# Kernel tuning notes

Measured on AMD Instinct MI355X. Metric: run time of the kernel, lower is better.

The kernel has to match this reference:

```python
import jax, jax.numpy as jnp
import numpy as np
import math

B, NV, L = 64, 21, 2048
PATCH, STRIDE = 16, 8
PNUM = (L - PATCH) // STRIDE + 1  # 255 patches
D, H, NDIM = 128, 256, 2
PRED = 96
EPS = 1e-5
SCALE = 1.0 / math.sqrt(NDIM)  # MultiHeadEMA scale = sqrt(1/ndim)
# patch gather indices: [PNUM, PATCH]
PIDX = np.arange(PNUM)[:, None] * STRIDE + np.arange(PATCH)[None, :]


def setup_inputs() -> dict:
    key = jax.random.key(0)
    ks = jax.random.split(key, 24)
    nrm = lambda k, shape, std: std * jax.random.normal(k, shape, jnp.float32)
    inp = {}
    inp['x'] = jax.random.normal(ks[0], (B, NV, L), jnp.float32)
    # LEMencoder feature_projection: LEMblock(PATCH -> H -> D)
    inp['fp_w1'] = nrm(ks[1], (PATCH, H), 0.1)
    inp['fp_b1'] = jnp.zeros((H,), jnp.float32)
    inp['fp_w2'] = nrm(ks[2], (H, D), 0.1)
    inp['fp_b2'] = jnp.zeros((D,), jnp.float32)
    inp['fp_wr'] = nrm(ks[3], (PATCH, D), 0.1)
    inp['fp_br'] = jnp.zeros((D,), jnp.float32)
    inp['fp_g'] = jnp.ones((D,), jnp.float32)
    inp['fp_be'] = jnp.zeros((D,), jnp.float32)
    # 2 stacked encoder LEMblocks (D -> D -> D), leading layer axis
    inp['enc_w1'] = nrm(ks[4], (2, D, D), 0.05)
    inp['enc_b1'] = jnp.zeros((2, D), jnp.float32)
    inp['enc_w2'] = nrm(ks[5], (2, D, D), 0.05)
    inp['enc_b2'] = jnp.zeros((2, D), jnp.float32)
    inp['enc_wr'] = nrm(ks[6], (2, D, D), 0.05)
    inp['enc_br'] = jnp.zeros((2, D), jnp.float32)
    inp['enc_g'] = jnp.ones((2, D), jnp.float32)
    inp['enc_be'] = jnp.zeros((2, D), jnp.float32)
    # MultiHeadEMA params (unidirectional: kernel_dim == D)
    inp['ema_delta'] = nrm(ks[7], (D, NDIM, 1), 0.2)
    inp['ema_alpha'] = nrm(ks[8], (D, NDIM, 1), 0.2)
    val = jnp.array([1.0, -1.0], jnp.float32).reshape(1, NDIM, 1)  # +1/-1 alternating init
    inp['ema_beta'] = nrm(ks[9], (D, NDIM, 1), 0.02) + val
    inp['ema_gamma'] = nrm(ks[10], (D, NDIM), 1.0)
    inp['ema_omega'] = nrm(ks[11], (D,), 1.0)
    # Flatten_Head (shared): Linear(D*PNUM -> PRED)
    inp['head_w'] = nrm(ks[12], (D * PNUM, PRED), 0.02)
    inp['head_b'] = jnp.zeros((PRED,), jnp.float32)
    return inp


def _lemblock(x, w1, b1, w2, b2, wr, br, g, be):
    h = jax.nn.relu(x @ w1 + b1) @ w2 + b2
    y = h + (x @ wr + br)
    mu = jnp.mean(y, axis=-1, keepdims=True)
    var = jnp.mean(jnp.square(y - mu), axis=-1, keepdims=True)
    return g * (y - mu) * jax.lax.rsqrt(var + EPS) + be


def reference(x, fp_w1, fp_b1, fp_w2, fp_b2, fp_wr, fp_br, fp_g, fp_be,
              enc_w1, enc_b1, enc_w2, enc_b2, enc_wr, enc_br, enc_g, enc_be,
              ema_delta, ema_alpha, ema_beta, ema_gamma, ema_omega,
              head_w, head_b):
    # patching: [B, NV, L] -> [B*NV, PNUM, PATCH]
    z = x[:, :, PIDX].reshape(B * NV, PNUM, PATCH)
    # LEMencoder
    z = _lemblock(z, fp_w1, fp_b1, fp_w2, fp_b2, fp_wr, fp_br, fp_g, fp_be)
    for i in range(enc_w1.shape[0]):
        z = _lemblock(z, enc_w1[i], enc_b1[i], enc_w2[i], enc_b2[i],
                      enc_wr[i], enc_br[i], enc_g[i], enc_be[i])
    # MultiHeadEMA over patch (time) axis; input [Time=PNUM, Batch=B*NV, Channel=D]
    t = jnp.transpose(z, (1, 0, 2))
    residual = t * ema_omega
    xc = jnp.transpose(t, (1, 2, 0))  # [BN, D, PNUM]
    p = jax.nn.sigmoid(ema_delta)           # [D, N, 1]
    q = 1.0 - p * jax.nn.sigmoid(ema_alpha)  # [D, N, 1]
    vander = jnp.arange(PNUM, dtype=jnp.float32)[None, None, :] * jnp.log(q)  # [D, N, PNUM]
    kern = p * ema_beta * jnp.exp(vander)
    k = jnp.einsum('dnl,dn->dl', kern, ema_gamma * SCALE)  # [D, PNUM]
    n2 = 2 * PNUM
    out = jnp.fft.irfft(jnp.fft.rfft(xc, n=n2) * jnp.fft.rfft(k, n=n2), n=n2)[..., :PNUM]
    out = jax.nn.silu(jnp.transpose(out, (2, 0, 1)) + residual)  # [PNUM, BN, D]
    # Flatten_Head (shared): [B, NV, D, PNUM] -> flatten(-2) -> linear
    u = jnp.transpose(out, (1, 2, 0)).reshape(B, NV, D * PNUM)
    return u @ head_w + head_b  # [B, NV, PRED]
```

## Files before the change

kernel.cpp:

```cpp
#include <hip/hip_runtime.h>

typedef unsigned short u16;
typedef short bf8v __attribute__((ext_vector_type(8)));
typedef float f4v __attribute__((ext_vector_type(4)));
typedef float f16v __attribute__((ext_vector_type(16)));

#define DEV static __device__ __forceinline__

constexpr int BB   = 64;
constexpr int NV   = 21;
constexpr int BN   = BB * NV;
constexpr int PNUM = 255;
constexpr int D    = 128;
constexpr int PRED = 96;
constexpr int ROWS = BN * PNUM;
constexpr int KH   = D * PNUM;
constexpr int CH   = 30;
constexpr int KPC  = KH / CH;
constexpr int HITER = KPC / 32;
constexpr float EMA_SCALE = 0.70710678118654752440f;

DEV float bf2f(u16 h) { return __uint_as_float(((unsigned)h) << 16); }
DEV u16 f2bf(float f) {
  unsigned u = __float_as_uint(f);
  return (u16)((u + 0x7fffu + ((u >> 16) & 1u)) >> 16);
}
DEV unsigned pkbf2(float a, float b) {
  unsigned ua = __float_as_uint(a) + 0x8000u;
  unsigned ub = __float_as_uint(b) + 0x8000u;
  return __builtin_amdgcn_perm(ub, ua, 0x07060302u);
}
DEV bf8v mk4(unsigned a, unsigned b, unsigned c, unsigned d) {
  int4 t = {(int)a, (int)b, (int)c, (int)d};
  bf8v r;
  __builtin_memcpy(&r, &t, 16);
  return r;
}
DEV bf8v ld8(const u16* p) {
  bf8v r;
  __builtin_memcpy(&r, p, 16);
  return r;
}
DEV f4v mfma16(bf8v a, bf8v b, f4v c) {
  return __builtin_amdgcn_mfma_f32_16x16x32_bf16(a, b, c, 0, 0, 0);
}
DEV f16v mfma32(bf8v a, bf8v b, f16v c) {
  return __builtin_amdgcn_mfma_f32_32x32x16_bf16(a, b, c, 0, 0, 0);
}
DEV f16v zero16() {
  f16v r;
#pragma unroll
  for (int i = 0; i < 16; i++) r[i] = 0.f;
  return r;
}

DEV bf8v frag_pl(unsigned x0, unsigned y0, unsigned x1, unsigned y1) {
  asm("v_permlane32_swap_b32 %0, %1" : "+v"(x0), "+v"(y0));
  asm("v_permlane32_swap_b32 %0, %1" : "+v"(x1), "+v"(y1));
  return mk4(x0, x1, y0, y1);
}
#define FRAG_PL(pk, ks)                                                        \
  frag_pl(pk[(ks) >> 1][2 * ((ks) & 1)][0],                                    \
          pk[(ks) >> 1][2 * ((ks) & 1) + 1][0],                                \
          pk[(ks) >> 1][2 * ((ks) & 1)][1],                                    \
          pk[(ks) >> 1][2 * ((ks) & 1) + 1][1])

__global__ void swz_all(
    const float* __restrict__ fw1, const float* __restrict__ fw2,
    const float* __restrict__ fwr, const float* __restrict__ ew1,
    const float* __restrict__ ew2, const float* __restrict__ ewr,
    const float* __restrict__ hw, u16* __restrict__ wb, u16* __restrict__ wsh) {
  int b = blockIdx.x;
  if (b >= 560) {
    int i = (b - 560) * 256 + threadIdx.x;
    if (i >= KH * PRED) return;
    int kp = i / PRED, n = i - kp * PRED;
    int l = kp >> 7, d = kp & 127;
    wsh[((size_t)(kp >> 3) * PRED + n) * 8 + (kp & 7)] =
        f2bf(hw[(size_t)(d * PNUM + l) * PRED + n]);
    return;
  }
  const float* src; u16* dst; int K, N, Kp;
  if (b < 32)       { src = fw1; dst = wb;          K = 16;  N = 256; Kp = 32; }
  else if (b < 160) { b -= 32;  src = fw2; dst = wb + 8192;  K = 256; N = 128; Kp = 256; }
  else if (b < 176) { b -= 160; src = fwr; dst = wb + 40960; K = 16;  N = 128; Kp = 32; }
  else {
    int e = (b - 176) >> 6; b = (b - 176) & 63;
    int l = e / 3, w = e - 3 * l;
    const float* basep = (w == 0) ? ew1 : (w == 1) ? ew2 : ewr;
    src = basep + (size_t)l * 16384;
    dst = wb + 45056 + e * 16384;
    K = 128; N = 128; Kp = 128;
  }
  int i = b * 256 + threadIdx.x;
  if (i >= Kp * N) return;
  int k = i / N, n = i - k * N;
  u16 v = (k < K) ? f2bf(src[(size_t)k * N + n]) : (u16)0;
  dst[((size_t)(k >> 3) * N + n) * 8 + (k & 7)] = v;
}

__global__ __launch_bounds__(128, 2) void k_lem(
    const float* __restrict__ x,
    const u16* __restrict__ ws1, const float* __restrict__ b1,
    const u16* __restrict__ ws2, const u16* __restrict__ wsr,
    const float* __restrict__ b2, const float* __restrict__ br,
    const float* __restrict__ g, const float* __restrict__ be,
    const u16* __restrict__ wse, const float* __restrict__ eb1,
    const float* __restrict__ eb2, const float* __restrict__ ebr,
    const float* __restrict__ eg, const float* __restrict__ ebe,
    u16* __restrict__ zout) {
  __shared__ __align__(16) u16 zst[64 * 132];
  const int t = threadIdx.x;
  const int lane = t & 63, w = t >> 6;
  const int hh = lane >> 5, r5 = lane & 31;
  const int tile = blockIdx.x;
  const int row = tile * 64 + w * 32 + r5;

  bf8v azv;
  {
    unsigned R = (unsigned)row;
    unsigned bn = R / 255u;
    unsigned p = R - bn * 255u;
    const float* px = x + (size_t)bn * 2048u + p * 8u + hh * 8;
    float4 v0 = *(const float4*)px;
    float4 v1 = *(const float4*)(px + 4);
    azv = mk4(pkbf2(v0.x, v0.y), pkbf2(v0.z, v0.w),
              pkbf2(v1.x, v1.y), pkbf2(v1.z, v1.w));
  }

  unsigned hpk[8][4][2];
  unsigned zpk[4][4][2];

#pragma unroll
  for (int half = 0; half < 2; half++) {
    f16v a[4];
#pragma unroll
    for (int gg = 0; gg < 4; gg++) {
      bf8v wf = ld8(ws1 + ((size_t)(hh * 256 + (half * 4 + gg) * 32 + r5)) * 8);
      a[gg] = mfma32(wf, azv, zero16());
    }
#pragma unroll
    for (int gg = 0; gg < 4; gg++)
#pragma unroll
      for (int wq = 0; wq < 4; wq++) {
        int c0 = (half * 4 + gg) * 32 + wq * 8 + 4 * hh;
        float4 bv = *(const float4*)(b1 + c0);
        float v0 = fmaxf(a[gg][wq * 4 + 0] + bv.x, 0.f);
        float v1 = fmaxf(a[gg][wq * 4 + 1] + bv.y, 0.f);
        float v2 = fmaxf(a[gg][wq * 4 + 2] + bv.z, 0.f);
        float v3 = fmaxf(a[gg][wq * 4 + 3] + bv.w, 0.f);
        hpk[half * 4 + gg][wq][0] = pkbf2(v0, v1);
        hpk[half * 4 + gg][wq][1] = pkbf2(v2, v3);
      }
  }

  {
    f16v acc[4];
#pragma unroll
    for (int gg = 0; gg < 4; gg++) acc[gg] = zero16();
    bf8v wq[3][4];
#pragma unroll
    for (int gg = 0; gg < 4; gg++)
      wq[0][gg] = ld8(wsr + ((size_t)(hh * 128 + gg * 32 + r5)) * 8);
#pragma unroll
    for (int gg = 0; gg < 4; gg++)
      wq[1][gg] = ld8(ws2 + ((size_t)(hh * 128 + gg * 32 + r5)) * 8);
    bf8v bf_cur = azv;
#pragma unroll
    for (int s = 0; s < 17; s++) {
      if (s + 2 < 17) {
        int ks = s + 1;
#pragma unroll
        for (int gg = 0; gg < 4; gg++)
          wq[(s + 2) % 3][gg] =
              ld8(ws2 + ((size_t)((2 * ks + hh) * 128 + gg * 32 + r5)) * 8);
      }
      bf8v bf_nxt = bf_cur;
      if (s + 1 < 17) bf_nxt = FRAG_PL(hpk, s);
#pragma unroll
      for (int gg = 0; gg < 4; gg++) acc[gg] = mfma32(wq[s % 3][gg], bf_cur, acc[gg]);
      bf_cur = bf_nxt;
    }
    float s = 0.f, s2 = 0.f;
#pragma unroll
    for (int gg = 0; gg < 4; gg++)
#pragma unroll
      for (int wq4 = 0; wq4 < 4; wq4++) {
        int c0 = gg * 32 + wq4 * 8 + 4 * hh;
        float4 bv2 = *(const float4*)(b2 + c0);
        float4 bvr = *(const float4*)(br + c0);
        acc[gg][wq4 * 4 + 0] += bv2.x + bvr.x;
        acc[gg][wq4 * 4 + 1] += bv2.y + bvr.y;
        acc[gg][wq4 * 4 + 2] += bv2.z + bvr.z;
        acc[gg][wq4 * 4 + 3] += bv2.w + bvr.w;
#pragma unroll
        for (int sidx = 0; sidx < 4; sidx++) {
          float v = acc[gg][wq4 * 4 + sidx];
          s += v; s2 += v * v;
        }
      }
    s += __shfl_xor(s, 32, 64); s2 += __shfl_xor(s2, 32, 64);
    float mean = s * (1.f / 128.f);
    float rstd = rsqrtf(s2 * (1.f / 128.f) - mean * mean + 1e-5f);
#pragma unroll
    for (int gg = 0; gg < 4; gg++)
#pragma unroll
      for (int wq4 = 0; wq4 < 4; wq4++) {
        int c0 = gg * 32 + wq4 * 8 + 4 * hh;
        float4 gv = *(const float4*)(g + c0);
        float4 bv = *(const float4*)(be + c0);
        float v0 = (acc[gg][wq4 * 4 + 0] - mean) * rstd * gv.x + bv.x;
        float v1 = (acc[gg][wq4 * 4 + 1] - mean) * rstd * gv.y + bv.y;
        float v2 = (acc[gg][wq4 * 4 + 2] - mean) * rstd * gv.z + bv.z;
        float v3 = (acc[gg][wq4 * 4 + 3] - mean) * rstd * gv.w + bv.w;
        zpk[gg][wq4][0] = pkbf2(v0, v1);
        zpk[gg][wq4][1] = pkbf2(v2, v3);
      }
  }

#pragma unroll 1
  for (int L = 0; L < 2; L++) {
    const u16* w1p = wse + (size_t)(L * 3 + 0) * 16384;
    const u16* w2p = wse + (size_t)(L * 3 + 1) * 16384;
    const u16* wrp = wse + (size_t)(L * 3 + 2) * 16384;
    unsigned hp2[4][4][2];
    {
      f16v a2[4];
#pragma unroll
      for (int gg = 0; gg < 4; gg++) a2[gg] = zero16();
      bf8v wq[3][4];
#pragma unroll
      for (int gg = 0; gg < 4; gg++)
        wq[0][gg] = ld8(w1p + ((size_t)(hh * 128 + gg * 32 + r5)) * 8);
#pragma unroll
      for (int gg = 0; gg < 4; gg++)
        wq[1][gg] = ld8(w1p + ((size_t)((2 + hh) * 128 + gg * 32 + r5)) * 8);
      bf8v bf_cur = FRAG_PL(zpk, 0);
#pragma unroll
      for (int s = 0; s < 8; s++) {
        if (s + 2 < 8) {
#pragma unroll
          for (int gg = 0; gg < 4; gg++)
            wq[(s + 2) % 3][gg] =
                ld8(w1p + ((size_t)((2 * (s + 2) + hh) * 128 + gg * 32 + r5)) * 8);
        }
        bf8v bf_nxt = bf_cur;
        if (s + 1 < 8) bf_nxt = FRAG_PL(zpk, s + 1);
#pragma unroll
        for (int gg = 0; gg < 4; gg++) a2[gg] = mfma32(wq[s % 3][gg], bf_cur, a2[gg]);
        bf_cur = bf_nxt;
      }
#pragma unroll
      for (int gg = 0; gg < 4; gg++)
#pragma unroll
        for (int wq4 = 0; wq4 < 4; wq4++) {
          int c0 = gg * 32 + wq4 * 8 + 4 * hh;
          float4 bv = *(const float4*)(eb1 + L * 128 + c0);
          float v0 = fmaxf(a2[gg][wq4 * 4 + 0] + bv.x, 0.f);
          float v1 = fmaxf(a2[gg][wq4 * 4 + 1] + bv.y, 0.f);
          float v2 = fmaxf(a2[gg][wq4 * 4 + 2] + bv.z, 0.f);
          float v3 = fmaxf(a2[gg][wq4 * 4 + 3] + bv.w, 0.f);
          hp2[gg][wq4][0] = pkbf2(v0, v1);
          hp2[gg][wq4][1] = pkbf2(v2, v3);
        }
    }
    f16v acc[4];
#pragma unroll
    for (int gg = 0; gg < 4; gg++) acc[gg] = zero16();
    {
      bf8v wq[3][4];
#pragma unroll
      for (int gg = 0; gg < 4; gg++)
        wq[0][gg] = ld8(w2p + ((size_t)(hh * 128 + gg * 32 + r5)) * 8);
#pragma unroll
      for (int gg = 0; gg < 4; gg++)
        wq[1][gg] = ld8(w2p + ((size_t)((2 + hh) * 128 + gg * 32 + r5)) * 8);
      bf8v bf_cur = FRAG_PL(hp2, 0);
#pragma unroll
      for (int s = 0; s < 16; s++) {
        if (s + 2 < 16) {
          int k2 = s + 2;
          const u16* wp = (k2 < 8) ? w2p : wrp;
          int kk = (k2 < 8) ? k2 : k2 - 8;
#pragma unroll
          for (int gg = 0; gg < 4; gg++)
            wq[k2 % 3][gg] =
                ld8(wp + ((size_t)((2 * kk + hh) * 128 + gg * 32 + r5)) * 8);
        }
        bf8v bf_nxt = bf_cur;
        if (s + 1 < 16) {
          int k1 = s + 1;
          bf_nxt = (k1 < 8) ? FRAG_PL(hp2, k1) : FRAG_PL(zpk, k1 - 8);
        }
#pragma unroll
        for (int gg = 0; gg < 4; gg++) acc[gg] = mfma32(wq[s % 3][gg], bf_cur, acc[gg]);
        bf_cur = bf_nxt;
      }
    }
    float s = 0.f, s2 = 0.f;
#pragma unroll
    for (int gg = 0; gg < 4; gg++)
#pragma unroll
      for (int wq4 = 0; wq4 < 4; wq4++) {
        int c0 = gg * 32 + wq4 * 8 + 4 * hh;
        float4 bv2 = *(const float4*)(eb2 + L * 128 + c0);
        float4 bvr = *(const float4*)(ebr + L * 128 + c0);
        acc[gg][wq4 * 4 + 0] += bv2.x + bvr.x;
        acc[gg][wq4 * 4 + 1] += bv2.y + bvr.y;
        acc[gg][wq4 * 4 + 2] += bv2.z + bvr.z;
        acc[gg][wq4 * 4 + 3] += bv2.w + bvr.w;
#pragma unroll
        for (int sidx = 0; sidx < 4; sidx++) {
          float v = acc[gg][wq4 * 4 + sidx];
          s += v; s2 += v * v;
        }
      }
    s += __shfl_xor(s, 32, 64); s2 += __shfl_xor(s2, 32, 64);
    float mean = s * (1.f / 128.f);
    float rstd = rsqrtf(s2 * (1.f / 128.f) - mean * mean + 1e-5f);
#pragma unroll
    for (int gg = 0; gg < 4; gg++)
#pragma unroll
      for (int wq4 = 0; wq4 < 4; wq4++) {
        int c0 = gg * 32 + wq4 * 8 + 4 * hh;
        float4 gv = *(const float4*)(eg + L * 128 + c0);
        float4 bv = *(const float4*)(ebe + L * 128 + c0);
        float v0 = (acc[gg][wq4 * 4 + 0] - mean) * rstd * gv.x + bv.x;
        float v1 = (acc[gg][wq4 * 4 + 1] - mean) * rstd * gv.y + bv.y;
        float v2 = (acc[gg][wq4 * 4 + 2] - mean) * rstd * gv.z + bv.z;
        float v3 = (acc[gg][wq4 * 4 + 3] - mean) * rstd * gv.w + bv.w;
        unsigned plo = pkbf2(v0, v1), phi = pkbf2(v2, v3);
        if (L == 0) {
          zpk[gg][wq4][0] = plo;
          zpk[gg][wq4][1] = phi;
        } else {
          uint2 pv = {plo, phi};
          *(uint2*)(zst + (w * 32 + r5) * 132 + c0) = pv;
        }
      }
  }

#pragma unroll
  for (int it = 0; it < 8; it++) {
    int lu = it * 64 + lane;
    int rr = lu >> 4, seg = lu & 15;
    int orow = w * 32 + rr;
    *(uint4*)(zout + ((size_t)tile * 64 + orow) * 128 + seg * 8) =
        *(const uint4*)(zst + orow * 132 + seg * 8);
  }
}

__global__ __launch_bounds__(128) void k_ema(
    u16* __restrict__ z,
    const float* __restrict__ pdel, const float* __restrict__ palp,
    const float* __restrict__ pbet, const float* __restrict__ pgam,
    const float* __restrict__ pome) {
  __shared__ __align__(16) u16 zc[64 * 128];
  const int t = threadIdx.x;
  const int bn = blockIdx.x;
  float p0 = 1.f / (1.f + __expf(-pdel[t * 2 + 0]));
  float p1 = 1.f / (1.f + __expf(-pdel[t * 2 + 1]));
  float q0 = 1.f - p0 / (1.f + __expf(-palp[t * 2 + 0]));
  float q1 = 1.f - p1 / (1.f + __expf(-palp[t * 2 + 1]));
  float w0 = p0 * pbet[t * 2 + 0] * pgam[t * 2 + 0] * EMA_SCALE;
  float w1 = p1 * pbet[t * 2 + 1] * pgam[t * 2 + 1] * EMA_SCALE;
  float om = pome[t];
  float s0 = 0.f, s1 = 0.f;
  u16* slab = z + (size_t)bn * KH;

  for (int ch = 0; ch < 4; ch++) {
    int nrow = (ch < 3) ? 64 : 63;
    int nval = nrow * 128;
    for (int i = t * 8; i < nval; i += 128 * 8)
      *(uint4*)(zc + i) = *(const uint4*)(slab + ch * 8192 + i);
    __syncthreads();
    for (int j0 = 0; j0 < nrow; j0 += 8) {
      float xs[8];
#pragma unroll
      for (int jj = 0; jj < 8; jj++)
        if (j0 + jj < nrow) xs[jj] = bf2f(zc[(j0 + jj) * 128 + t]);
#pragma unroll
      for (int jj = 0; jj < 8; jj++)
        if (j0 + jj < nrow) {
          float xv = xs[jj];
          s0 = q0 * s0 + xv;
          s1 = q1 * s1 + xv;
          float v = w0 * s0 + w1 * s1 + om * xv;
          xs[jj] = v / (1.f + __expf(-v));
        }
#pragma unroll
      for (int jj = 0; jj < 8; jj++)
        if (j0 + jj < nrow)
          zc[(j0 + jj) * 128 + t] = (u16)((__float_as_uint(xs[jj]) + 0x8000u) >> 16);
    }
    __syncthreads();
    for (int i = t * 8; i < nval; i += 128 * 8)
      *(uint4*)(slab + ch * 8192 + i) = *(const uint4*)(zc + i);
    __syncthreads();
  }
}

__global__ __launch_bounds__(256) void k_head(
    const u16* __restrict__ u, const u16* __restrict__ whs, float* __restrict__ part) {
  const int t = threadIdx.x;
  const int lane = t & 63, wid = t >> 6;
  const int quad = lane >> 4, lc = lane & 15;
  const int tile = blockIdx.x;
  const int ch = blockIdx.y;
  const int m0 = tile * 64 + wid * 16;
  const u16* Ab = u + (size_t)(m0 + lc) * KH + (size_t)ch * KPC;
  const int g0 = ch * (KPC / 8);
  f4v acc[6];
#pragma unroll
  for (int n = 0; n < 6; n++) acc[n] = (f4v){0.f, 0.f, 0.f, 0.f};
  bf8v a_nxt = ld8(Ab + quad * 8);
  bf8v b_nxt[6];
#pragma unroll
  for (int n = 0; n < 6; n++)
    b_nxt[n] = ld8(whs + ((size_t)(g0 + quad) * PRED + n * 16 + lc) * 8);
  for (int ks = 0; ks < HITER; ks++) {
    bf8v a_cur = a_nxt;
    bf8v b_cur[6];
#pragma unroll
    for (int n = 0; n < 6; n++) b_cur[n] = b_nxt[n];
    if (ks < HITER - 1) {
      a_nxt = ld8(Ab + (ks + 1) * 32 + quad * 8);
#pragma unroll
      for (int n = 0; n < 6; n++)
        b_nxt[n] = ld8(whs + ((size_t)(g0 + (ks + 1) * 4 + quad) * PRED + n * 16 + lc) * 8);
    }
#pragma unroll
    for (int n = 0; n < 6; n++) acc[n] = mfma16(a_cur, b_cur[n], acc[n]);
  }
#pragma unroll
  for (int n = 0; n < 6; n++) {
    int col = n * 16 + lc;
#pragma unroll
    for (int r = 0; r < 4; r++)
      part[((size_t)ch * BN + m0 + quad * 4 + r) * PRED + col] = acc[n][r];
  }
}

__global__ __launch_bounds__(256) void k_red(
    const float* __restrict__ part, const float* __restrict__ hb, float* __restrict__ out) {
  int i = blockIdx.x * 256 + threadIdx.x;
  if (i >= BN * PRED) return;
  int row = i / PRED, col = i - row * PRED;
  float s = hb[col];
#pragma unroll 5
  for (int c = 0; c < CH; c++) s += part[((size_t)c * BN + row) * PRED + col];
  out[i] = s;
}

extern "C" void kernel_launch(void* const* d_in, const int* in_sizes, int n_in,
                              void* d_out, int out_size, void* d_ws, size_t ws_size,
                              hipStream_t stream) {
  const float* x      = (const float*)d_in[0];
  const float* fp_w1  = (const float*)d_in[1];
  const float* fp_b1  = (const float*)d_in[2];
  const float* fp_w2  = (const float*)d_in[3];
  const float* fp_b2  = (const float*)d_in[4];
  const float* fp_wr  = (const float*)d_in[5];
  const float* fp_br  = (const float*)d_in[6];
  const float* fp_g   = (const float*)d_in[7];
  const float* fp_be  = (const float*)d_in[8];
  const float* enc_w1 = (const float*)d_in[9];
  const float* enc_b1 = (const float*)d_in[10];
  const float* enc_w2 = (const float*)d_in[11];
  const float* enc_b2 = (const float*)d_in[12];
  const float* enc_wr = (const float*)d_in[13];
  const float* enc_br = (const float*)d_in[14];
  const float* enc_g  = (const float*)d_in[15];
  const float* enc_be = (const float*)d_in[16];
  const float* e_del  = (const float*)d_in[17];
  const float* e_alp  = (const float*)d_in[18];
  const float* e_bet  = (const float*)d_in[19];
  const float* e_gam  = (const float*)d_in[20];
  const float* e_om   = (const float*)d_in[21];
  const float* head_w = (const float*)d_in[22];
  const float* head_b = (const float*)d_in[23];

  char* base = (char*)d_ws;
  u16* z3 = (u16*)base;
  const size_t EZB = (size_t)ROWS * 128 * 2;
  float* part = (float*)(base + EZB);
  const size_t PARTB = (size_t)CH * BN * PRED * 4;
  u16* wb = (u16*)(base + EZB + PARTB);
  u16* ws1 = wb;
  u16* ws2 = wb + 8192;
  u16* wsr = wb + 40960;
  u16* wse = wb + 45056;
  u16* wsh = wb + 143360;

  swz_all<<<560 + (KH * PRED + 255) / 256, 256, 0, stream>>>(
      fp_w1, fp_w2, fp_wr, enc_w1, enc_w2, enc_wr, head_w, wb, wsh);

  k_lem<<<ROWS / 64, 128, 0, stream>>>(x, ws1, fp_b1, ws2, wsr, fp_b2, fp_br, fp_g, fp_be,
                                       wse, enc_b1, enc_b2, enc_br, enc_g, enc_be, z3);
  k_ema<<<BN, 128, 0, stream>>>(z3, e_del, e_alp, e_bet, e_gam, e_om);
  k_head<<<dim3(21, CH), 256, 0, stream>>>(z3, wsh, part);
  k_red<<<(BN * PRED + 255) / 256, 256, 0, stream>>>(part, head_b, (float*)d_out);
}
```

Before: 397.5 us.

## Stream hidden activations through MLP chunks to cut registers and raise occupancy

Reorders each LEM block so that the first-layer hidden activations are computed one 32-column chunk at a time and fed straight into the second GEMM. The full hidden tile no longer has to stay in registers, and the residual projection is issued first into the shared accumulator. This lets launch bounds rise from 2 to 3 blocks per CU. LayerNorm reductions now use partial sums combined through permlane32 swaps instead of shuffles. The trade-off is that the triple-buffered weight prefetch pipeline is gone, so load latency is exposed more directly.

Measured after the change: 528.3 us. 32.9% more time.

```diff
diff --git a/kernel.cpp b/kernel.cpp
--- a/kernel.cpp
+++ b/kernel.cpp
@@ -59,11 +59,12 @@
   asm("v_permlane32_swap_b32 %0, %1" : "+v"(x1), "+v"(y1));
   return mk4(x0, x1, y0, y1);
 }
-#define FRAG_PL(pk, ks)                                                        \
-  frag_pl(pk[(ks) >> 1][2 * ((ks) & 1)][0],                                    \
-          pk[(ks) >> 1][2 * ((ks) & 1) + 1][0],                                \
-          pk[(ks) >> 1][2 * ((ks) & 1)][1],                                    \
-          pk[(ks) >> 1][2 * ((ks) & 1) + 1][1])
+
+DEV float xadd32(float v) {
+  unsigned a = __float_as_uint(v), b = a;
+  asm("v_permlane32_swap_b32 %0, %1" : "+v"(a), "+v"(b));
+  return __uint_as_float(a) + __uint_as_float(b);
+}
 
 __global__ void swz_all(
     const float* __restrict__ fw1, const float* __restrict__ fw2,
@@ -99,7 +100,7 @@
   dst[((size_t)(k >> 3) * N + n) * 8 + (k & 7)] = v;
 }
 
-__global__ __launch_bounds__(128, 2) void k_lem(
+__global__ __launch_bounds__(128, 3) void k_lem(
     const float* __restrict__ x,
     const u16* __restrict__ ws1, const float* __restrict__ b1,
     const u16* __restrict__ ws2, const u16* __restrict__ wsr,
@@ -128,62 +129,49 @@
               pkbf2(v1.x, v1.y), pkbf2(v1.z, v1.w));
   }
 
-  unsigned hpk[8][4][2];
+  f16v acc[4];
   unsigned zpk[4][4][2];
-
-#pragma unroll
-  for (int half = 0; half < 2; half++) {
-    f16v a[4];
+  bf8v zfr[8];
+
+  {
+#pragma unroll
+    for (int gg = 0; gg < 4; gg++)
+      acc[gg] = mfma32(ld8(wsr + ((size_t)(hh * 128 + gg * 32 + r5)) * 8), azv,
+                       zero16());
+#pragma unroll
+    for (int gq = 0; gq < 8; gq++) {
+      bf8v w2x[4], w2y[4];
+#pragma unroll
+      for (int gg = 0; gg < 4; gg++)
+        w2x[gg] = ld8(ws2 + ((size_t)((4 * gq + hh) * 128 + gg * 32 + r5)) * 8);
+#pragma unroll
+      for (int gg = 0; gg < 4; gg++)
+        w2y[gg] = ld8(ws2 + ((size_t)((4 * gq + 2 + hh) * 128 + gg * 32 + r5)) * 8);
+      bf8v w1f = ld8(ws1 + ((size_t)(hh * 256 + gq * 32 + r5)) * 8);
+      f16v hv = mfma32(w1f, azv, zero16());
+      unsigned hq[4][2];
+#pragma unroll
+      for (int wq = 0; wq < 4; wq++) {
+        int c0 = gq * 32 + wq * 8 + 4 * hh;
+        float4 bv = *(const float4*)(b1 + c0);
+        float v0 = fmaxf(hv[wq * 4 + 0] + bv.x, 0.f);
+        float v1 = fmaxf(hv[wq * 4 + 1] + bv.y, 0.f);
+        float v2 = fmaxf(hv[wq * 4 + 2] + bv.z, 0.f);
+        float v3 = fmaxf(hv[wq * 4 + 3] + bv.w, 0.f);
+        hq[wq][0] = pkbf2(v0, v1);
+        hq[wq][1] = pkbf2(v2, v3);
+      }
+      bf8v f0 = frag_pl(hq[0][0], hq[1][0], hq[0][1], hq[1][1]);
+      bf8v f1 = frag_pl(hq[2][0], hq[3][0], hq[2][1], hq[3][1]);
+#pragma unroll
+      for (int gg = 0; gg < 4; gg++) acc[gg] = mfma32(w2x[gg], f0, acc[gg]);
+#pragma unroll
+      for (int gg = 0; gg < 4; gg++) acc[gg] = mfma32(w2y[gg], f1, acc[gg]);
+    }
+    float sa[4], qa[4];
 #pragma unroll
     for (int gg = 0; gg < 4; gg++) {
-      bf8v wf = ld8(ws1 + ((size_t)(hh * 256 + (half * 4 + gg) * 32 + r5)) * 8);
-      a[gg] = mfma32(wf, azv, zero16());
-    }
-#pragma unroll
-    for (int gg = 0; gg < 4; gg++)
-#pragma unroll
-      for (int wq = 0; wq < 4; wq++) {
-        int c0 = (half * 4 + gg) * 32 + wq * 8 + 4 * hh;
-        float4 bv = *(const float4*)(b1 + c0);
-        float v0 = fmaxf(a[gg][wq * 4 + 0] + bv.x, 0.f);
-        float v1 = fmaxf(a[gg][wq * 4 + 1] + bv.y, 0.f);
-        float v2 = fmaxf(a[gg][wq * 4 + 2] + bv.z, 0.f);
-        float v3 = fmaxf(a[gg][wq * 4 + 3] + bv.w, 0.f);
-        hpk[half * 4 + gg][wq][0] = pkbf2(v0, v1);
-        hpk[half * 4 + gg][wq][1] = pkbf2(v2, v3);
-      }
-  }
-
-  {
-    f16v acc[4];
-#pragma unroll
-    for (int gg = 0; gg < 4; gg++) acc[gg] = zero16();
-    bf8v wq[3][4];
-#pragma unroll
-    for (int gg = 0; gg < 4; gg++)
-      wq[0][gg] = ld8(wsr + ((size_t)(hh * 128 + gg * 32 + r5)) * 8);
-#pragma unroll
-    for (int gg = 0; gg < 4; gg++)
-      wq[1][gg] = ld8(ws2 + ((size_t)(hh * 128 + gg * 32 + r5)) * 8);
-    bf8v bf_cur = azv;
-#pragma unroll
-    for (int s = 0; s < 17; s++) {
-      if (s + 2 < 17) {
-        int ks = s + 1;
-#pragma unroll
-        for (int gg = 0; gg < 4; gg++)
-          wq[(s + 2) % 3][gg] =
-              ld8(ws2 + ((size_t)((2 * ks + hh) * 128 + gg * 32 + r5)) * 8);
-      }
-      bf8v bf_nxt = bf_cur;
-      if (s + 1 < 17) bf_nxt = FRAG_PL(hpk, s);
-#pragma unroll
-      for (int gg = 0; gg < 4; gg++) acc[gg] = mfma32(wq[s % 3][gg], bf_cur, acc[gg]);
-      bf_cur = bf_nxt;
-    }
-    float s = 0.f, s2 = 0.f;
-#pragma unroll
-    for (int gg = 0; gg < 4; gg++)
+      float s = 0.f, q = 0.f;
 #pragma unroll
       for (int wq4 = 0; wq4 < 4; wq4++) {
         int c0 = gg * 32 + wq4 * 8 + 4 * hh;
@@ -196,12 +184,15 @@
 #pragma unroll
         for (int sidx = 0; sidx < 4; sidx++) {
           float v = acc[gg][wq4 * 4 + sidx];
-          s += v; s2 += v * v;
+          s += v; q += v * v;
         }
       }
-    s += __shfl_xor(s, 32, 64); s2 += __shfl_xor(s2, 32, 64);
+      sa[gg] = s; qa[gg] = q;
+    }
+    float s = xadd32((sa[0] + sa[1]) + (sa[2] + sa[3]));
+    float q = xadd32((qa[0] + qa[1]) + (qa[2] + qa[3]));
     float mean = s * (1.f / 128.f);
-    float rstd = rsqrtf(s2 * (1.f / 128.f) - mean * mean + 1e-5f);
+    float rstd = rsqrtf(q * (1.f / 128.f) - mean * mean + 1e-5f);
 #pragma unroll
     for (int gg = 0; gg < 4; gg++)
 #pragma unroll
@@ -223,83 +214,60 @@
     const u16* w1p = wse + (size_t)(L * 3 + 0) * 16384;
     const u16* w2p = wse + (size_t)(L * 3 + 1) * 16384;
     const u16* wrp = wse + (size_t)(L * 3 + 2) * 16384;
-    unsigned hp2[4][4][2];
-    {
-      f16v a2[4];
-#pragma unroll
-      for (int gg = 0; gg < 4; gg++) a2[gg] = zero16();
-      bf8v wq[3][4];
+#pragma unroll
+    for (int gq = 0; gq < 4; gq++) {
+      zfr[2 * gq] =
+          frag_pl(zpk[gq][0][0], zpk[gq][1][0], zpk[gq][0][1], zpk[gq][1][1]);
+      zfr[2 * gq + 1] =
+          frag_pl(zpk[gq][2][0], zpk[gq][3][0], zpk[gq][2][1], zpk[gq][3][1]);
+    }
+#pragma unroll
+    for (int gg = 0; gg < 4; gg++) acc[gg] = zero16();
+#pragma unroll
+    for (int ks = 0; ks < 8; ks++)
+#pragma unroll
+      for (int gg = 0; gg < 4; gg++) {
+        bf8v wf = ld8(wrp + ((size_t)((2 * ks + hh) * 128 + gg * 32 + r5)) * 8);
+        acc[gg] = mfma32(wf, zfr[ks], acc[gg]);
+      }
+#pragma unroll
+    for (int gq = 0; gq < 4; gq++) {
+      bf8v w2x[4], w2y[4];
 #pragma unroll
       for (int gg = 0; gg < 4; gg++)
-        wq[0][gg] = ld8(w1p + ((size_t)(hh * 128 + gg * 32 + r5)) * 8);
+        w2x[gg] = ld8(w2p + ((size_t)((4 * gq + hh) * 128 + gg * 32 + r5)) * 8);
 #pragma unroll
       for (int gg = 0; gg < 4; gg++)
-        wq[1][gg] = ld8(w1p + ((size_t)((2 + hh) * 128 + gg * 32 + r5)) * 8);
-      bf8v bf_cur = FRAG_PL(zpk, 0);
-#pragma unroll
-      for (int s = 0; s < 8; s++) {
-        if (s + 2 < 8) {
-#pragma unroll
-          for (int gg = 0; gg < 4; gg++)
-            wq[(s + 2) % 3][gg] =
-                ld8(w1p + ((size_t)((2 * (s + 2) + hh) * 128 + gg * 32 + r5)) * 8);
-        }
-        bf8v bf_nxt = bf_cur;
-        if (s + 1 < 8) bf_nxt = FRAG_PL(zpk, s + 1);
-#pragma unroll
-        for (int gg = 0; gg < 4; gg++) a2[gg] = mfma32(wq[s % 3][gg], bf_cur, a2[gg]);
-        bf_cur = bf_nxt;
-      }
-#pragma unroll
-      for (int gg = 0; gg < 4; gg++)
-#pragma unroll
-        for (int wq4 = 0; wq4 < 4; wq4++) {
-          int c0 = gg * 32 + wq4 * 8 + 4 * hh;
-          float4 bv = *(const float4*)(eb1 + L * 128 + c0);
-          float v0 = fmaxf(a2[gg][wq4 * 4 + 0] + bv.x, 0.f);
-          float v1 = fmaxf(a2[gg][wq4 * 4 + 1] + bv.y, 0.f);
-          float v2 = fmaxf(a2[gg][wq4 * 4 + 2] + bv.z, 0.f);
-          float v3 = fmaxf(a2[gg][wq4 * 4 + 3] + bv.w, 0.f);
-          hp2[gg][wq4][0] = pkbf2(v0, v1);
-          hp2[gg][wq4][1] = pkbf2(v2, v3);
-        }
-    }
-    f16v acc[4];
-#pragma unroll
-    for (int gg = 0; gg < 4; gg++) acc[gg] = zero16();
-    {
-      bf8v wq[3][4];
-#pragma unroll
-      for (int gg = 0; gg < 4; gg++)
-        wq[0][gg] = ld8(w2p + ((size_t)(hh * 128 + gg * 32 + r5)) * 8);
-#pragma unroll
-      for (int gg = 0; gg < 4; gg++)
-        wq[1][gg] = ld8(w2p + ((size_t)((2 + hh) * 128 + gg * 32 + r5)) * 8);
-      bf8v bf_cur = FRAG_PL(hp2, 0);
-#pragma unroll
-      for (int s = 0; s < 16; s++) {
-        if (s + 2 < 16) {
-          int k2 = s + 2;
-          const u16* wp = (k2 < 8) ? w2p : wrp;
-          int kk = (k2 < 8) ? k2 : k2 - 8;
-#pragma unroll
-          for (int gg = 0; gg < 4; gg++)
-            wq[k2 % 3][gg] =
-                ld8(wp + ((size_t)((2 * kk + hh) * 128 + gg * 32 + r5)) * 8);
-        }
-        bf8v bf_nxt = bf_cur;
-        if (s + 1 < 16) {
-          int k1 = s + 1;
-          bf_nxt = (k1 < 8) ? FRAG_PL(hp2, k1) : FRAG_PL(zpk, k1 - 8);
-        }
-#pragma unroll
-        for (int gg = 0; gg < 4; gg++) acc[gg] = mfma32(wq[s % 3][gg], bf_cur, acc[gg]);
-        bf_cur = bf_nxt;
-      }
-    }
-    float s = 0.f, s2 = 0.f;
-#pragma unroll
-    for (int gg = 0; gg < 4; gg++)
+        w2y[gg] = ld8(w2p + ((size_t)((4 * gq + 2 + hh) * 128 + gg * 32 + r5)) * 8);
+      f16v av = zero16();
+#pragma unroll
+      for (int ks = 0; ks < 8; ks++) {
+        bf8v wf = ld8(w1p + ((size_t)((2 * ks + hh) * 128 + gq * 32 + r5)) * 8);
+        av = mfma32(wf, zfr[ks], av);
+      }
+      unsigned hq[4][2];
+#pragma unroll
+      for (int wq = 0; wq < 4; wq++) {
+        int c0 = gq * 32 + wq * 8 + 4 * hh;
+        float4 bv = *(const float4*)(eb1 + L * 128 + c0);
+        float v0 = fmaxf(av[wq * 4 + 0] + bv.x, 0.f);
+        float v1 = fmaxf(av[wq * 4 + 1] + bv.y, 0.f);
+        float v2 = fmaxf(av[wq * 4 + 2] + bv.z, 0.f);
+        float v3 = fmaxf(av[wq * 4 + 3] + bv.w, 0.f);
+        hq[wq][0] = pkbf2(v0, v1);
+        hq[wq][1] = pkbf2(v2, v3);
+      }
+      bf8v f0 = frag_pl(hq[0][0], hq[1][0], hq[0][1], hq[1][1]);
+      bf8v f1 = frag_pl(hq[2][0], hq[3][0], hq[2][1], hq[3][1]);
+#pragma unroll
+      for (int gg = 0; gg < 4; gg++) acc[gg] = mfma32(w2x[gg], f0, acc[gg]);
+#pragma unroll
+      for (int gg = 0; gg < 4; gg++) acc[gg] = mfma32(w2y[gg], f1, acc[gg]);
+    }
+    float sa[4], qa[4];
+#pragma unroll
+    for (int gg = 0; gg < 4; gg++) {
+      float s = 0.f, q = 0.f;
 #pragma unroll
       for (int wq4 = 0; wq4 < 4; wq4++) {
         int c0 = gg * 32 + wq4 * 8 + 4 * hh;
@@ -312,12 +280,15 @@
 #pragma unroll
         for (int sidx = 0; sidx < 4; sidx++) {
           float v = acc[gg][wq4 * 4 + sidx];
-          s += v; s2 += v * v;
+          s += v; q += v * v;
         }
       }
-    s += __shfl_xor(s, 32, 64); s2 += __shfl_xor(s2, 32, 64);
+      sa[gg] = s; qa[gg] = q;
+    }
+    float s = xadd32((sa[0] + sa[1]) + (sa[2] + sa[3]));
+    float q = xadd32((qa[0] + qa[1]) + (qa[2] + qa[3]));
     float mean = s * (1.f / 128.f);
-    float rstd = rsqrtf(s2 * (1.f / 128.f) - mean * mean + 1e-5f);
+    float rstd = rsqrtf(q * (1.f / 128.f) - mean * mean + 1e-5f);
 #pragma unroll
     for (int gg = 0; gg < 4; gg++)
 #pragma unroll
```
